# Kernel optimization log

Hardware: AMD Instinct MI355X
Metric: run time of the kernel (lower is better)

Reference implementation:

```python
import jax, jax.numpy as jnp
import numpy as np

VOCAB, EMB = 100000, 50
KERNEL_NUM, SIGMA, EXACT_SIGMA = 21, 0.1, 0.001
OUT_LAYERS = [10, 5]


def _kernel_params():
    # Mirrors KNRM._get_kernels_layers
    mus = [1.0]
    bin_size = 2.0 / (KERNEL_NUM - 1)
    mus.append(1 - bin_size / 2)
    for i in range(1, KERNEL_NUM - 1):
        mus.append(mus[i] - bin_size)
    mus = list(reversed(mus))
    sigmas = [SIGMA] * (KERNEL_NUM - 1) + [EXACT_SIGMA]
    return np.array(mus, np.float32), np.array(sigmas, np.float32)

MUS, SIGMAS = _kernel_params()


def setup_inputs() -> dict:
    key = jax.random.key(0)
    ks = jax.random.split(key, 12)
    B, LQ, LD = 2048, 32, 256
    emb = jax.random.normal(ks[0], (VOCAB, EMB), jnp.float32)
    emb = emb.at[0].set(0.0)  # padding_idx=0
    query1 = jax.random.randint(ks[1], (B, LQ), 0, VOCAB)
    doc1 = jax.random.randint(ks[2], (B, LD), 0, VOCAB)
    query2 = jax.random.randint(ks[3], (B, LQ), 0, VOCAB)
    doc2 = jax.random.randint(ks[4], (B, LD), 0, VOCAB)
    def lin(k, fan_in, fan_out):
        bound = 1.0 / np.sqrt(fan_in)
        kw, kb = jax.random.split(k)
        w = jax.random.uniform(kw, (fan_out, fan_in), jnp.float32, -bound, bound)
        b = jax.random.uniform(kb, (fan_out,), jnp.float32, -bound, bound)
        return w, b
    w0, b0 = lin(ks[5], KERNEL_NUM, OUT_LAYERS[0])
    w1, b1 = lin(ks[6], OUT_LAYERS[0], OUT_LAYERS[1])
    w2, b2 = lin(ks[7], OUT_LAYERS[1], 1)
    return dict(emb=emb, w0=w0, b0=b0, w1=w1, b1=b1, w2=w2, b2=b2,
                query1=query1, doc1=doc1, query2=query2, doc2=doc2)


def _matching_matrix(emb, query, doc):
    qe = emb[query]                     # [B, Lq, E]
    de = emb[doc]                       # [B, Ld, E]
    qn = qe / (jnp.linalg.norm(qe, axis=-1, keepdims=True) + 1e-13)
    dn = de / (jnp.linalg.norm(de, axis=-1, keepdims=True) + 1e-13)
    return jnp.einsum('bqe,bde->bqd', qn, dn)  # cosine sim [B, Lq, Ld]


def _apply_kernels(mm):
    # Loop over the fixed 21 kernels (structurally distinct mu/sigma),
    # avoiding a [B,Lq,Ld,21] intermediate, as the original does.
    km = []
    for mu, sg in zip(MUS, SIGMAS):
        k = jnp.exp(-(mm - mu) ** 2 / (2.0 * sg * sg))
        km.append(jnp.log1p(k.sum(axis=-1)).sum(axis=-1))  # [B]
    return jnp.stack(km, axis=1)  # [B, K]


def _mlp(x, w0, b0, w1, b1, w2, b2):
    h = jax.nn.relu(x @ w0.T + b0)
    h = jax.nn.relu(h @ w1.T + b1)
    return h @ w2.T + b2  # [B, 1]


def _predict(emb, w0, b0, w1, b1, w2, b2, query, doc):
    mm = _matching_matrix(emb, query, doc)
    ko = _apply_kernels(mm)
    return _mlp(ko, w0, b0, w1, b1, w2, b2)


def reference(emb, w0, b0, w1, b1, w2, b2, query1, doc1, query2, doc2):
    logits1 = _predict(emb, w0, b0, w1, b1, w2, b2, query1, doc1)
    logits2 = _predict(emb, w0, b0, w1, b1, w2, b2, query2, doc2)
    return jax.nn.sigmoid(logits1 - logits2)  # [B, 1]
```

## Files before the change

### kernel.cpp

```cpp
#include <hip/hip_runtime.h>

#define EMB_N 50
#define KP 64
#define LQ 32
#define LD 256
#define KN 21
#define BATCH 2048
#define VROWS 64

typedef short v8s __attribute__((ext_vector_type(8)));
typedef float v4f __attribute__((ext_vector_type(4)));
typedef float v2f __attribute__((ext_vector_type(2)));

#define PK_ACC(d, b)     asm("v_pk_add_f32 %0, %0, %1" : "+v"(d) : "v"(b))
#define PK_MULA(d, b)    asm("v_pk_mul_f32 %0, %0, %1" : "+v"(d) : "v"(b))
#define PK_FMA(d, a, b)  asm("v_pk_fma_f32 %0, %1, %2, %0" : "+v"(d) : "v"(a), "v"(b))

__device__ inline short bf16_rne(float f) {
  unsigned u = __float_as_uint(f);
  unsigned r = u + 0x7fffu + ((u >> 16) & 1u);
  return (short)(r >> 16);
}
__device__ inline float bf16_tof(short h) {
  return __uint_as_float(((unsigned)(unsigned short)h) << 16);
}

__global__ __launch_bounds__(512) void vocab_norm_kernel(
    const float* __restrict__ emb, short* __restrict__ vb,
    short* __restrict__ vlo, int vocab)
{
  __shared__ float lds[VROWS * EMB_N];
  const int tid = threadIdx.x;
  const long long ftotal = (long long)vocab * EMB_N;
  const long long fbase  = (long long)blockIdx.x * (VROWS * EMB_N);

  const float4* e4 = (const float4*)emb;
#pragma unroll
  for (int i = 0; i < 2; i++) {
    int idx = i * 512 + tid;
    if (idx < (VROWS * EMB_N) / 4) {
      long long g4 = fbase / 4 + idx;
      if (g4 * 4 + 3 < ftotal) {
        *(float4*)&lds[idx * 4] = e4[g4];
      } else {
#pragma unroll
        for (int k = 0; k < 4; k++) {
          long long gf = g4 * 4 + k;
          lds[idx * 4 + k] = (gf < ftotal) ? emb[gf] : 0.f;
        }
      }
    }
  }
  __syncthreads();

  const int r = tid >> 3;
  const int c = tid & 7;
  const int row = blockIdx.x * VROWS + r;
  if (row >= vocab) return;

  float v[8];
#pragma unroll
  for (int k = 0; k < 8; k++) v[k] = 0.f;
  float ss = 0.f;
  const int e0 = c * 8;
  const int cnt = (c < 6) ? 8 : (c == 6 ? 2 : 0);
  for (int k = 0; k < cnt; k++) {
    float t = lds[r * EMB_N + e0 + k];
    v[k] = t;
    ss = fmaf(t, t, ss);
  }
  ss += __shfl_xor(ss, 1);
  ss += __shfl_xor(ss, 2);
  ss += __shfl_xor(ss, 4);
  float inv = 1.0f / (sqrtf(ss) + 1e-13f);
  short hi[8], lo[8];
#pragma unroll
  for (int k = 0; k < 8; k++) {
    float f = v[k] * inv;
    hi[k] = bf16_rne(f);
    lo[k] = bf16_rne(f - bf16_tof(hi[k]));
  }
  size_t o = (size_t)row * KP + e0;
  *(uint4*)(vb + o)  = *(const uint4*)hi;
  *(uint4*)(vlo + o) = *(const uint4*)lo;
}

__device__ __constant__ const float CJ[KN] = {
  2.5261639e-20f, 2.0469719e-16f, 6.1019363e-13f, 6.6915861e-10f, 2.6995785e-7f,
  4.0065297e-5f,  2.1874911e-3f,  4.3936937e-2f,  0.32465247f,    0.88249690f,
  0.88249690f,    0.32465247f,    4.3936937e-2f,  2.1874911e-3f,  4.0065297e-5f,
  2.6995785e-7f,  6.6915861e-10f, 6.1019363e-13f, 2.0469719e-16f, 2.5261639e-20f,
  1.0f
};

__global__ __launch_bounds__(256, 6) void knrm_main_kernel(
    const short* __restrict__ vb, const short* __restrict__ vlo,
    const int* __restrict__ q1, const int* __restrict__ d1,
    const int* __restrict__ q2, const int* __restrict__ d2,
    const float* __restrict__ w0, const float* __restrict__ b0,
    const float* __restrict__ w1, const float* __restrict__ b1,
    const float* __restrict__ w2, const float* __restrict__ b2,
    float* __restrict__ lgbuf)
{
  __shared__ float part[4][16][KN];
  __shared__ float Sqex[LQ];
  __shared__ float ko[KN];
  __shared__ float h0s[10];
  __shared__ float h1s[5];

  const int pair = blockIdx.x >> 11;
  const int b = blockIdx.x & (BATCH - 1);
  const int tid = threadIdx.x;
  const int wave = tid >> 6;
  const int lane = tid & 63;
  const int l15 = lane & 15;
  const int quad = lane >> 4;
  const int qtile = wave >> 1;
  const int thalf = wave & 1;

  const int* qp = pair ? q2 : q1;
  const int* dp = pair ? d2 : d1;

  if (tid < LQ) Sqex[tid] = 0.f;

  int qtok = qp[b * LQ + qtile * 16 + l15];
  const short* qh = vb  + (size_t)qtok * KP + quad * 8;
  const short* ql = vlo + (size_t)qtok * KP + quad * 8;
  v8s Bh0 = *(const v8s*)(qh);
  v8s Bh1 = *(const v8s*)(qh + 32);
  v8s Bl0 = *(const v8s*)(ql);
  v8s Bl1 = *(const v8s*)(ql + 32);

  int mydtok = dp[b * LD + tid];

  __syncthreads();

#pragma unroll
  for (int qq = 0; qq < LQ; qq++) {
    int qt = qp[b * LQ + qq];
    unsigned long long m = __ballot(mydtok == qt && qt != 0);
    if (lane == 0 && m)
      atomicAdd(&Sqex[qq], (float)__popcll(m));
  }

  v2f U2[10];
#pragma unroll
  for (int i = 0; i < 10; i++) U2[i] = (v2f){0.f, 0.f};

#pragma unroll 1
  for (int t = 0; t < 8; t++) {
    int dtok = dp[b * LD + (thalf * 8 + t) * 16 + l15];
    const short* dptr = vb + (size_t)dtok * KP + quad * 8;
    v8s A0 = *(const v8s*)(dptr);
    v8s A1 = *(const v8s*)(dptr + 32);

    v4f C = {0.f, 0.f, 0.f, 0.f};
    C = __builtin_amdgcn_mfma_f32_16x16x32_bf16(A0, Bh0, C, 0, 0, 0);
    C = __builtin_amdgcn_mfma_f32_16x16x32_bf16(A1, Bh1, C, 0, 0, 0);
    C = __builtin_amdgcn_mfma_f32_16x16x32_bf16(A0, Bl0, C, 0, 0, 0);
    C = __builtin_amdgcn_mfma_f32_16x16x32_bf16(A1, Bl1, C, 0, 0, 0);

#pragma unroll
    for (int rp = 0; rp < 2; rp++) {
      v2f p0, p1, rr0, rr1;
      {
        float x = C[rp * 2];
        float gc = __builtin_amdgcn_exp2f(x * fmaf(-72.1347520f, x, 7.2134752f));
        float ex = 14.4269504f * x;
        float e1 = __builtin_amdgcn_exp2f(ex);
        float ei = __builtin_amdgcn_exp2f(-ex);
        p0 = (v2f){gc, gc * ei};  rr0 = (v2f){e1, ei};
      }
      {
        float x = C[rp * 2 + 1];
        float gc = __builtin_amdgcn_exp2f(x * fmaf(-72.1347520f, x, 7.2134752f));
        float ex = 14.4269504f * x;
        float e1 = __builtin_amdgcn_exp2f(ex);
        float ei = __builtin_amdgcn_exp2f(-ex);
        p1 = (v2f){gc, gc * ei};  rr1 = (v2f){e1, ei};
      }
      v2f s0 = rr0, s1 = rr1;
      PK_MULA(s0, rr0);
      PK_MULA(s1, rr1);
#pragma unroll
      for (int m = 0; m < 5; m++) {
        PK_ACC(U2[2 * m], p0);
        PK_FMA(U2[2 * m + 1], p0, rr0);
        if (m < 4) PK_MULA(p0, s0);
        PK_ACC(U2[2 * m], p1);
        PK_FMA(U2[2 * m + 1], p1, rr1);
        if (m < 4) PK_MULA(p1, s1);
      }
    }
  }

#pragma unroll
  for (int i = 0; i < 10; i++) {
    float ux = U2[i].x, uy = U2[i].y;
    ux += __shfl_xor(ux, 16);  uy += __shfl_xor(uy, 16);
    ux += __shfl_xor(ux, 32);  uy += __shfl_xor(uy, 32);
    if (quad == 0) {
      part[wave][l15][10 + i] = ux;
      part[wave][l15][9 - i]  = uy;
    }
  }
  __syncthreads();

  {
    int qq = tid & 31;
    int qi = qq & 15, qt2 = qq >> 4;
    int jb = tid >> 5;
#pragma unroll
    for (int k = 0; k < 3; k++) {
      int j = jb + 8 * k;
      float l = 0.f;
      if (j < KN) {
        float s = (j < 20) ? part[qt2 * 2][qi][j] + part[qt2 * 2 + 1][qi][j]
                           : Sqex[qq];
        float y = fmaf(CJ[j], s, 1.0f);
        l = 0.69314718f * __builtin_amdgcn_logf(y);
      }
      l += __shfl_xor(l, 1);  l += __shfl_xor(l, 2);
      l += __shfl_xor(l, 4);  l += __shfl_xor(l, 8);
      l += __shfl_xor(l, 16);
      if (qq == 0 && j < KN) ko[j] = l;
    }
  }
  __syncthreads();

  if (tid < 10) {
    float h = b0[tid];
#pragma unroll
    for (int k = 0; k < KN; k++) h = fmaf(w0[tid * KN + k], ko[k], h);
    h0s[tid] = fmaxf(h, 0.f);
  }
  __syncthreads();
  if (tid < 5) {
    float h = b1[tid];
#pragma unroll
    for (int k = 0; k < 10; k++) h = fmaf(w1[tid * 10 + k], h0s[k], h);
    h1s[tid] = fmaxf(h, 0.f);
  }
  __syncthreads();
  if (tid == 0) {
    float h = b2[0];
#pragma unroll
    for (int k = 0; k < 5; k++) h = fmaf(w2[k], h1s[k], h);
    lgbuf[pair * BATCH + b] = h;
  }
}

__global__ __launch_bounds__(256) void knrm_combine_kernel(
    const float* __restrict__ lgbuf, float* __restrict__ out)
{
  int i = blockIdx.x * 256 + threadIdx.x;
  if (i < BATCH) {
    float z = lgbuf[i] - lgbuf[BATCH + i];
    out[i] = 1.0f / (1.0f + expf(-z));
  }
}

extern "C" void kernel_launch(void* const* d_in, const int* in_sizes, int n_in,
                              void* d_out, int out_size, void* d_ws, size_t ws_size,
                              hipStream_t stream)
{
  const float* emb = (const float*)d_in[0];
  const float* w0  = (const float*)d_in[1];
  const float* b0  = (const float*)d_in[2];
  const float* w1  = (const float*)d_in[3];
  const float* b1  = (const float*)d_in[4];
  const float* w2  = (const float*)d_in[5];
  const float* b2  = (const float*)d_in[6];
  const int* q1 = (const int*)d_in[7];
  const int* dd1 = (const int*)d_in[8];
  const int* q2 = (const int*)d_in[9];
  const int* dd2 = (const int*)d_in[10];
  float* out = (float*)d_out;

  int vocab = in_sizes[0] / EMB_N;
  int B = in_sizes[7] / LQ;

  float* lgbuf = (float*)d_ws;
  short* vb  = (short*)(lgbuf + 2 * BATCH);
  short* vlo = vb + (size_t)vocab * KP;

  vocab_norm_kernel<<<(vocab + VROWS - 1) / VROWS, 512, 0, stream>>>(emb, vb, vlo, vocab);
  knrm_main_kernel<<<2 * B, 256, 0, stream>>>(vb, vlo, q1, dd1, q2, dd2,
                                              w0, b0, w1, b1, w2, b2, lgbuf);
  knrm_combine_kernel<<<(B + 255) / 256, 256, 0, stream>>>(lgbuf, out);
}
```

Measured before the change: 141.9 us.

## Fuse pair loop and sigmoid combine into main kernel, prefetch doc tiles

Each block now handles both query/doc pairs for one batch row in a sequential loop and writes the sigmoid of the logit difference directly. This removes the separate combine kernel and the logit workspace. The doc-token embedding loads for the next tile are software-prefetched into registers while the current tile's MFMA and kernel math run, and the launch-bounds occupancy hint drops from 6 to 5 to leave room for the extra registers. The cost is half as many blocks, each doing twice the work serially, which may reduce the parallelism available to hide latency.

```diff
diff --git a/kernel.cpp b/kernel.cpp
--- a/kernel.cpp
+++ b/kernel.cpp
@@ -93,14 +93,14 @@
   1.0f
 };
 
-__global__ __launch_bounds__(256, 6) void knrm_main_kernel(
+__global__ __launch_bounds__(256, 5) void knrm_main_kernel(
     const short* __restrict__ vb, const short* __restrict__ vlo,
     const int* __restrict__ q1, const int* __restrict__ d1,
     const int* __restrict__ q2, const int* __restrict__ d2,
     const float* __restrict__ w0, const float* __restrict__ b0,
     const float* __restrict__ w1, const float* __restrict__ b1,
     const float* __restrict__ w2, const float* __restrict__ b2,
-    float* __restrict__ lgbuf)
+    float* __restrict__ out)
 {
   __shared__ float part[4][16][KN];
   __shared__ float Sqex[LQ];
@@ -108,8 +108,7 @@
   __shared__ float h0s[10];
   __shared__ float h1s[5];
 
-  const int pair = blockIdx.x >> 11;
-  const int b = blockIdx.x & (BATCH - 1);
+  const int b = blockIdx.x;
   const int tid = threadIdx.x;
   const int wave = tid >> 6;
   const int lane = tid & 63;
@@ -118,146 +117,154 @@
   const int qtile = wave >> 1;
   const int thalf = wave & 1;
 
-  const int* qp = pair ? q2 : q1;
-  const int* dp = pair ? d2 : d1;
-
-  if (tid < LQ) Sqex[tid] = 0.f;
-
-  int qtok = qp[b * LQ + qtile * 16 + l15];
-  const short* qh = vb  + (size_t)qtok * KP + quad * 8;
-  const short* ql = vlo + (size_t)qtok * KP + quad * 8;
-  v8s Bh0 = *(const v8s*)(qh);
-  v8s Bh1 = *(const v8s*)(qh + 32);
-  v8s Bl0 = *(const v8s*)(ql);
-  v8s Bl1 = *(const v8s*)(ql + 32);
-
-  int mydtok = dp[b * LD + tid];
-
-  __syncthreads();
-
-#pragma unroll
-  for (int qq = 0; qq < LQ; qq++) {
-    int qt = qp[b * LQ + qq];
-    unsigned long long m = __ballot(mydtok == qt && qt != 0);
-    if (lane == 0 && m)
-      atomicAdd(&Sqex[qq], (float)__popcll(m));
-  }
-
-  v2f U2[10];
-#pragma unroll
-  for (int i = 0; i < 10; i++) U2[i] = (v2f){0.f, 0.f};
+  float z = 0.f;
 
 #pragma unroll 1
-  for (int t = 0; t < 8; t++) {
-    int dtok = dp[b * LD + (thalf * 8 + t) * 16 + l15];
-    const short* dptr = vb + (size_t)dtok * KP + quad * 8;
+  for (int pair = 0; pair < 2; pair++) {
+    const int* qp = pair ? q2 : q1;
+    const int* dp = pair ? d2 : d1;
+
+    __syncthreads();
+    if (tid < LQ) Sqex[tid] = 0.f;
+
+    int qtok = qp[b * LQ + qtile * 16 + l15];
+    const short* qh = vb  + (size_t)qtok * KP + quad * 8;
+    const short* ql = vlo + (size_t)qtok * KP + quad * 8;
+    v8s Bh0 = *(const v8s*)(qh);
+    v8s Bh1 = *(const v8s*)(qh + 32);
+    v8s Bl0 = *(const v8s*)(ql);
+    v8s Bl1 = *(const v8s*)(ql + 32);
+
+    int mydtok = dp[b * LD + tid];
+
+    __syncthreads();
+
+#pragma unroll
+    for (int qq = 0; qq < LQ; qq++) {
+      int qt = qp[b * LQ + qq];
+      unsigned long long m = __ballot(mydtok == qt && qt != 0);
+      if (lane == 0 && m)
+        atomicAdd(&Sqex[qq], (float)__popcll(m));
+    }
+
+    v2f U2[10];
+#pragma unroll
+    for (int i = 0; i < 10; i++) U2[i] = (v2f){0.f, 0.f};
+
+    int dtok0 = dp[b * LD + (thalf * 8) * 16 + l15];
+    const short* dptr = vb + (size_t)dtok0 * KP + quad * 8;
     v8s A0 = *(const v8s*)(dptr);
     v8s A1 = *(const v8s*)(dptr + 32);
 
-    v4f C = {0.f, 0.f, 0.f, 0.f};
-    C = __builtin_amdgcn_mfma_f32_16x16x32_bf16(A0, Bh0, C, 0, 0, 0);
-    C = __builtin_amdgcn_mfma_f32_16x16x32_bf16(A1, Bh1, C, 0, 0, 0);
-    C = __builtin_amdgcn_mfma_f32_16x16x32_bf16(A0, Bl0, C, 0, 0, 0);
-    C = __builtin_amdgcn_mfma_f32_16x16x32_bf16(A1, Bl1, C, 0, 0, 0);
-
-#pragma unroll
-    for (int rp = 0; rp < 2; rp++) {
-      v2f p0, p1, rr0, rr1;
-      {
-        float x = C[rp * 2];
-        float gc = __builtin_amdgcn_exp2f(x * fmaf(-72.1347520f, x, 7.2134752f));
-        float ex = 14.4269504f * x;
-        float e1 = __builtin_amdgcn_exp2f(ex);
-        float ei = __builtin_amdgcn_exp2f(-ex);
-        p0 = (v2f){gc, gc * ei};  rr0 = (v2f){e1, ei};
-      }
-      {
-        float x = C[rp * 2 + 1];
-        float gc = __builtin_amdgcn_exp2f(x * fmaf(-72.1347520f, x, 7.2134752f));
-        float ex = 14.4269504f * x;
-        float e1 = __builtin_amdgcn_exp2f(ex);
-        float ei = __builtin_amdgcn_exp2f(-ex);
-        p1 = (v2f){gc, gc * ei};  rr1 = (v2f){e1, ei};
-      }
-      v2f s0 = rr0, s1 = rr1;
-      PK_MULA(s0, rr0);
-      PK_MULA(s1, rr1);
-#pragma unroll
-      for (int m = 0; m < 5; m++) {
-        PK_ACC(U2[2 * m], p0);
-        PK_FMA(U2[2 * m + 1], p0, rr0);
-        if (m < 4) PK_MULA(p0, s0);
-        PK_ACC(U2[2 * m], p1);
-        PK_FMA(U2[2 * m + 1], p1, rr1);
-        if (m < 4) PK_MULA(p1, s1);
-      }
-    }
-  }
-
-#pragma unroll
-  for (int i = 0; i < 10; i++) {
-    float ux = U2[i].x, uy = U2[i].y;
-    ux += __shfl_xor(ux, 16);  uy += __shfl_xor(uy, 16);
-    ux += __shfl_xor(ux, 32);  uy += __shfl_xor(uy, 32);
-    if (quad == 0) {
-      part[wave][l15][10 + i] = ux;
-      part[wave][l15][9 - i]  = uy;
-    }
-  }
-  __syncthreads();
-
-  {
-    int qq = tid & 31;
-    int qi = qq & 15, qt2 = qq >> 4;
-    int jb = tid >> 5;
-#pragma unroll
-    for (int k = 0; k < 3; k++) {
-      int j = jb + 8 * k;
-      float l = 0.f;
-      if (j < KN) {
-        float s = (j < 20) ? part[qt2 * 2][qi][j] + part[qt2 * 2 + 1][qi][j]
-                           : Sqex[qq];
-        float y = fmaf(CJ[j], s, 1.0f);
-        l = 0.69314718f * __builtin_amdgcn_logf(y);
-      }
-      l += __shfl_xor(l, 1);  l += __shfl_xor(l, 2);
-      l += __shfl_xor(l, 4);  l += __shfl_xor(l, 8);
-      l += __shfl_xor(l, 16);
-      if (qq == 0 && j < KN) ko[j] = l;
-    }
-  }
-  __syncthreads();
-
-  if (tid < 10) {
-    float h = b0[tid];
-#pragma unroll
-    for (int k = 0; k < KN; k++) h = fmaf(w0[tid * KN + k], ko[k], h);
-    h0s[tid] = fmaxf(h, 0.f);
-  }
-  __syncthreads();
-  if (tid < 5) {
-    float h = b1[tid];
-#pragma unroll
-    for (int k = 0; k < 10; k++) h = fmaf(w1[tid * 10 + k], h0s[k], h);
-    h1s[tid] = fmaxf(h, 0.f);
-  }
-  __syncthreads();
-  if (tid == 0) {
-    float h = b2[0];
-#pragma unroll
-    for (int k = 0; k < 5; k++) h = fmaf(w2[k], h1s[k], h);
-    lgbuf[pair * BATCH + b] = h;
-  }
-}
-
-__global__ __launch_bounds__(256) void knrm_combine_kernel(
-    const float* __restrict__ lgbuf, float* __restrict__ out)
-{
-  int i = blockIdx.x * 256 + threadIdx.x;
-  if (i < BATCH) {
-    float z = lgbuf[i] - lgbuf[BATCH + i];
-    out[i] = 1.0f / (1.0f + expf(-z));
-  }
+#pragma unroll 1
+    for (int t = 0; t < 8; t++) {
+      v8s N0, N1;
+      if (t < 7) {
+        int ndtok = dp[b * LD + (thalf * 8 + t + 1) * 16 + l15];
+        const short* nptr = vb + (size_t)ndtok * KP + quad * 8;
+        N0 = *(const v8s*)(nptr);
+        N1 = *(const v8s*)(nptr + 32);
+      }
+
+      v4f C = {0.f, 0.f, 0.f, 0.f};
+      C = __builtin_amdgcn_mfma_f32_16x16x32_bf16(A0, Bh0, C, 0, 0, 0);
+      C = __builtin_amdgcn_mfma_f32_16x16x32_bf16(A1, Bh1, C, 0, 0, 0);
+      C = __builtin_amdgcn_mfma_f32_16x16x32_bf16(A0, Bl0, C, 0, 0, 0);
+      C = __builtin_amdgcn_mfma_f32_16x16x32_bf16(A1, Bl1, C, 0, 0, 0);
+
+#pragma unroll
+      for (int rp = 0; rp < 2; rp++) {
+        v2f p0, p1, rr0, rr1;
+        {
+          float x = C[rp * 2];
+          float gc = __builtin_amdgcn_exp2f(x * fmaf(-72.1347520f, x, 7.2134752f));
+          float ex = 14.4269504f * x;
+          float e1 = __builtin_amdgcn_exp2f(ex);
+          float ei = __builtin_amdgcn_exp2f(-ex);
+          p0 = (v2f){gc, gc * ei};  rr0 = (v2f){e1, ei};
+        }
+        {
+          float x = C[rp * 2 + 1];
+          float gc = __builtin_amdgcn_exp2f(x * fmaf(-72.1347520f, x, 7.2134752f));
+          float ex = 14.4269504f * x;
+          float e1 = __builtin_amdgcn_exp2f(ex);
+          float ei = __builtin_amdgcn_exp2f(-ex);
+          p1 = (v2f){gc, gc * ei};  rr1 = (v2f){e1, ei};
+        }
+        v2f s0 = rr0, s1 = rr1;
+        PK_MULA(s0, rr0);
+        PK_MULA(s1, rr1);
+#pragma unroll
+        for (int m = 0; m < 5; m++) {
+          PK_ACC(U2[2 * m], p0);
+          PK_FMA(U2[2 * m + 1], p0, rr0);
+          if (m < 4) PK_MULA(p0, s0);
+          PK_ACC(U2[2 * m], p1);
+          PK_FMA(U2[2 * m + 1], p1, rr1);
+          if (m < 4) PK_MULA(p1, s1);
+        }
+      }
+      if (t < 7) { A0 = N0; A1 = N1; }
+    }
+
+#pragma unroll
+    for (int i = 0; i < 10; i++) {
+      float ux = U2[i].x, uy = U2[i].y;
+      ux += __shfl_xor(ux, 16);  uy += __shfl_xor(uy, 16);
+      ux += __shfl_xor(ux, 32);  uy += __shfl_xor(uy, 32);
+      if (quad == 0) {
+        part[wave][l15][10 + i] = ux;
+        part[wave][l15][9 - i]  = uy;
+      }
+    }
+    __syncthreads();
+
+    {
+      int qq = tid & 31;
+      int qi = qq & 15, qt2 = qq >> 4;
+      int jb = tid >> 5;
+#pragma unroll
+      for (int k = 0; k < 3; k++) {
+        int j = jb + 8 * k;
+        float l = 0.f;
+        if (j < KN) {
+          float s = (j < 20) ? part[qt2 * 2][qi][j] + part[qt2 * 2 + 1][qi][j]
+                             : Sqex[qq];
+          float y = fmaf(CJ[j], s, 1.0f);
+          l = 0.69314718f * __builtin_amdgcn_logf(y);
+        }
+        l += __shfl_xor(l, 1);  l += __shfl_xor(l, 2);
+        l += __shfl_xor(l, 4);  l += __shfl_xor(l, 8);
+        l += __shfl_xor(l, 16);
+        if (qq == 0 && j < KN) ko[j] = l;
+      }
+    }
+    __syncthreads();
+
+    if (tid < 10) {
+      float h = b0[tid];
+#pragma unroll
+      for (int k = 0; k < KN; k++) h = fmaf(w0[tid * KN + k], ko[k], h);
+      h0s[tid] = fmaxf(h, 0.f);
+    }
+    __syncthreads();
+    if (tid < 5) {
+      float h = b1[tid];
+#pragma unroll
+      for (int k = 0; k < 10; k++) h = fmaf(w1[tid * 10 + k], h0s[k], h);
+      h1s[tid] = fmaxf(h, 0.f);
+    }
+    __syncthreads();
+    if (tid == 0) {
+      float h = b2[0];
+#pragma unroll
+      for (int k = 0; k < 5; k++) h = fmaf(w2[k], h1s[k], h);
+      z = pair ? (z - h) : h;
+    }
+  }
+
+  if (tid == 0)
+    out[b] = 1.0f / (1.0f + __expf(-z));
 }
 
 extern "C" void kernel_launch(void* const* d_in, const int* in_sizes, int n_in,
@@ -280,12 +287,10 @@
   int vocab = in_sizes[0] / EMB_N;
   int B = in_sizes[7] / LQ;
 
-  float* lgbuf = (float*)d_ws;
-  short* vb  = (short*)(lgbuf + 2 * BATCH);
+  short* vb  = (short*)d_ws;
   short* vlo = vb + (size_t)vocab * KP;
 
   vocab_norm_kernel<<<(vocab + VROWS - 1) / VROWS, 512, 0, stream>>>(emb, vb, vlo, vocab);
-  knrm_main_kernel<<<2 * B, 256, 0, stream>>>(vb, vlo, q1, dd1, q2, dd2,
-                                              w0, b0, w1, b1, w2, b2, lgbuf);
-  knrm_combine_kernel<<<(B + 255) / 256, 256, 0, stream>>>(lgbuf, out);
-}
+  knrm_main_kernel<<<B, 256, 0, stream>>>(vb, vlo, q1, dd1, q2, dd2,
+                                          w0, b0, w1, b1, w2, b2, out);
+}
```

Result: slower. 157.1 us (+10.7%).
